# Kernel tuning notes

Measured on AMD Instinct MI355X. Metric: run time of the kernel, lower is better.

The kernel has to match this reference:

```python
import jax, jax.numpy as jnp
import numpy as np

B, C, G, S, R = 8192, 4096, 16, 256, 512  # batch, in_channels, clusters, cluster_size, j_rank


def setup_inputs() -> dict:
    key = jax.random.key(0)
    kx, kw, kb, kp = jax.random.split(key, 4)
    x = jax.random.normal(kx, (B, C), dtype=jnp.float32)
    # per-cluster Linear weights [G, out=R, in=S] and biases [G, R]
    W = jax.random.normal(kw, (G, R, S), dtype=jnp.float32) * (1.0 / np.sqrt(S))
    b = jax.random.normal(kb, (G, R), dtype=jnp.float32) * 0.01
    # arrangements: non-contiguous channel clusters = random permutation split into G groups
    perm = jax.random.permutation(kp, C).reshape(G, S).astype(jnp.int32)
    return {"x": x, "W": W, "b": b, "perm": perm}


def reference(x, W, b, perm):
    # gather each cluster's channels: [B, G, S]
    xg = x[:, perm]
    # batched per-cluster linear (y = x_c @ W_c^T + b_c), then concat along dim 1
    out = jnp.einsum('bgs,grs->bgr', xg, W) + b  # [B, G, R]
    return out.reshape(x.shape[0], G * R)
```

## Files before the change

### kernel.cpp

```cpp
#include <hip/hip_runtime.h>

#define BB 8192
#define CC 4096
#define GG 16
#define SS 256
#define RR 512
#define NN (GG*RR)

typedef __bf16 bf16x8 __attribute__((ext_vector_type(8)));
typedef float  f32x4_t __attribute__((ext_vector_type(4)));

__device__ __forceinline__ unsigned short f2bf(float f){
  union{float f; unsigned int u;} v; v.f = f;
  unsigned int r = (v.u + 0x7FFFu + ((v.u>>16)&1u)) >> 16;
  return (unsigned short)r;
}

__device__ __forceinline__ void gld_lds16(const void* g, void* l){
  __builtin_amdgcn_global_load_lds((const __attribute__((address_space(1))) void*)g,
                                   (__attribute__((address_space(3))) void*)l, 16, 0, 0);
}

__global__ void __launch_bounds__(256) permute_cast_kernel(
    const float* __restrict__ x, const int* __restrict__ perm,
    unsigned short* __restrict__ xp)
{
  __shared__ float row[CC];
  const int tid = threadIdx.x;
  const size_t b = blockIdx.x;
  const float4* xr = (const float4*)(x + b*CC);
  float4* rr = (float4*)row;
  #pragma unroll
  for (int c=0;c<4;++c) rr[c*256+tid] = xr[c*256+tid];
  __syncthreads();
  unsigned short* xo = xp + b*CC;
  #pragma unroll
  for (int c=0;c<2;++c){
    const int j0 = (((c<<8)+tid)<<3);
    const int* pp = perm + j0;
    unsigned int w0 = (unsigned)f2bf(row[pp[0]]) | ((unsigned)f2bf(row[pp[1]])<<16);
    unsigned int w1 = (unsigned)f2bf(row[pp[2]]) | ((unsigned)f2bf(row[pp[3]])<<16);
    unsigned int w2 = (unsigned)f2bf(row[pp[4]]) | ((unsigned)f2bf(row[pp[5]])<<16);
    unsigned int w3 = (unsigned)f2bf(row[pp[6]]) | ((unsigned)f2bf(row[pp[7]])<<16);
    uint4 o; o.x=w0; o.y=w1; o.z=w2; o.w=w3;
    *(uint4*)(xo + j0) = o;
  }
}

__global__ void __launch_bounds__(256) cast_w_kernel(
    const float* __restrict__ W, unsigned short* __restrict__ Wb)
{
  const int i = (blockIdx.x*256 + threadIdx.x)<<3;
  float4 f0 = ((const float4*)(W+i))[0];
  float4 f1 = ((const float4*)(W+i))[1];
  uint4 o;
  o.x = (unsigned)f2bf(f0.x) | ((unsigned)f2bf(f0.y)<<16);
  o.y = (unsigned)f2bf(f0.z) | ((unsigned)f2bf(f0.w)<<16);
  o.z = (unsigned)f2bf(f1.x) | ((unsigned)f2bf(f1.y)<<16);
  o.w = (unsigned)f2bf(f1.z) | ((unsigned)f2bf(f1.w)<<16);
  *(uint4*)(Wb+i) = o;
}

__global__ void __launch_bounds__(256) gemm_kernel(
    const unsigned short* __restrict__ xp, const unsigned short* __restrict__ Wb,
    const float* __restrict__ bias, float* __restrict__ out)
{
  __shared__ unsigned short lA[128*64];
  __shared__ unsigned short lB[128*64];
  const int tid  = threadIdx.x;
  const int lane = tid & 63;
  const int w    = tid >> 6;
  const int wr   = w >> 1, wc = w & 1;
  const int l15  = lane & 15, lh = lane >> 4;

  const int bid   = blockIdx.x;
  const int xcd   = bid & 7;
  const int local = bid >> 3;
  const int bx    = (xcd << 3) + (local & 7);
  const int by    = local >> 3;

  const int m0 = by << 7;
  const int n0 = bx << 7;
  const int g  = bx >> 2;
  const size_t arow0 = (size_t)m0*CC + (size_t)g*SS;
  const size_t brow0 = (size_t)n0*SS;

  f32x4_t acc[4][4];
  for (int i=0;i<4;++i)
    for (int j=0;j<4;++j)
      acc[i][j] = (f32x4_t){0.f,0.f,0.f,0.f};

  for (int kk=0; kk<SS; kk+=64){
    #pragma unroll
    for (int c=0;c<4;++c){
      const int i  = (c<<8) + tid;
      const int r  = i>>3;
      const int cs = ((i&7) ^ (r&7)) << 3;
      gld_lds16(xp + arow0 + (size_t)r*CC + kk + cs, &lA[i<<3]);
      gld_lds16(Wb + brow0 + (size_t)r*SS + kk + cs, &lB[i<<3]);
    }
    __syncthreads();
    #pragma unroll
    for (int ks=0;ks<2;++ks){
      bf16x8 af[4], bfr[4];
      const int cc = (ks<<2) + lh;
      #pragma unroll
      for (int mi=0;mi<4;++mi){
        const int ar = (wr<<6)+(mi<<4)+l15;
        af[mi]  = *(const bf16x8*)&lA[ar*64 + ((cc ^ (ar&7))<<3)];
      }
      #pragma unroll
      for (int ni=0;ni<4;++ni){
        const int br = (wc<<6)+(ni<<4)+l15;
        bfr[ni] = *(const bf16x8*)&lB[br*64 + ((cc ^ (br&7))<<3)];
      }
      #pragma unroll
      for (int mi=0;mi<4;++mi){
        #pragma unroll
        for (int ni=0;ni<4;++ni)
          acc[mi][ni] = __builtin_amdgcn_mfma_f32_16x16x32_bf16(af[mi], bfr[ni], acc[mi][ni], 0,0,0);
      }
    }
    __syncthreads();
  }

  #pragma unroll
  for (int ni=0;ni<4;++ni){
    const int col = n0 + (wc<<6) + (ni<<4) + l15;
    const float bv = bias[col];
    #pragma unroll
    for (int mi=0;mi<4;++mi){
      const int rb = m0 + (wr<<6) + (mi<<4) + (lh<<2);
      float* op = out + (size_t)rb*NN + col;
      #pragma unroll
      for (int r=0;r<4;++r)
        op[(size_t)r*NN] = acc[mi][ni][r] + bv;
    }
  }
}

extern "C" void kernel_launch(void* const* d_in, const int* in_sizes, int n_in,
                              void* d_out, int out_size, void* d_ws, size_t ws_size,
                              hipStream_t stream) {
  const float* x    = (const float*)d_in[0];
  const float* W    = (const float*)d_in[1];
  const float* bias = (const float*)d_in[2];
  const int*   perm = (const int*)d_in[3];
  float* out = (float*)d_out;

  unsigned short* xp = (unsigned short*)d_ws;
  unsigned short* Wb = (unsigned short*)((char*)d_ws + (size_t)BB*CC*2);

  permute_cast_kernel<<<dim3(BB), dim3(256), 0, stream>>>(x, perm, xp);
  cast_w_kernel<<<dim3((GG*RR*SS)/(256*8)), dim3(256), 0, stream>>>(W, Wb);
  gemm_kernel<<<dim3(4096), dim3(256), 0, stream>>>(xp, Wb, bias, out);
}
```

Measured before the change: 137.1 us.

## Double-buffer GEMM LDS tiles with 8 waves and merge prep kernels

Merges the x permute/cast and W cast kernels into one launch by splitting the block index range. The GEMM now uses 512 threads (8 waves, each with a 64x32 sub-tile) and double-buffered LDS, so direct-to-LDS loads for the next K step are issued while the current one computes, synchronised with explicit vmcnt waits and barriers. This aims to hide global load latency and cut one launch. The cost is twice the LDS per block and a fragile hand-counted vmcnt scheme.

Result: faster. 123.8 us (-9.6%).

```diff
diff --git a/kernel.cpp b/kernel.cpp
--- a/kernel.cpp
+++ b/kernel.cpp
@@ -21,56 +21,57 @@
                                    (__attribute__((address_space(3))) void*)l, 16, 0, 0);
 }
 
-__global__ void __launch_bounds__(256) permute_cast_kernel(
+__global__ void __launch_bounds__(256) prep_kernel(
     const float* __restrict__ x, const int* __restrict__ perm,
-    unsigned short* __restrict__ xp)
+    const float* __restrict__ W,
+    unsigned short* __restrict__ xp, unsigned short* __restrict__ Wb)
 {
   __shared__ float row[CC];
   const int tid = threadIdx.x;
-  const size_t b = blockIdx.x;
-  const float4* xr = (const float4*)(x + b*CC);
-  float4* rr = (float4*)row;
-  #pragma unroll
-  for (int c=0;c<4;++c) rr[c*256+tid] = xr[c*256+tid];
-  __syncthreads();
-  unsigned short* xo = xp + b*CC;
-  #pragma unroll
-  for (int c=0;c<2;++c){
-    const int j0 = (((c<<8)+tid)<<3);
-    const int* pp = perm + j0;
-    unsigned int w0 = (unsigned)f2bf(row[pp[0]]) | ((unsigned)f2bf(row[pp[1]])<<16);
-    unsigned int w1 = (unsigned)f2bf(row[pp[2]]) | ((unsigned)f2bf(row[pp[3]])<<16);
-    unsigned int w2 = (unsigned)f2bf(row[pp[4]]) | ((unsigned)f2bf(row[pp[5]])<<16);
-    unsigned int w3 = (unsigned)f2bf(row[pp[6]]) | ((unsigned)f2bf(row[pp[7]])<<16);
-    uint4 o; o.x=w0; o.y=w1; o.z=w2; o.w=w3;
-    *(uint4*)(xo + j0) = o;
+  const int bid = blockIdx.x;
+  if (bid < BB) {
+    const size_t b = bid;
+    const float4* xr = (const float4*)(x + b*CC);
+    float4* rr = (float4*)row;
+    #pragma unroll
+    for (int c=0;c<4;++c) rr[c*256+tid] = xr[c*256+tid];
+    __syncthreads();
+    unsigned short* xo = xp + b*CC;
+    #pragma unroll
+    for (int c=0;c<2;++c){
+      const int j0 = (((c<<8)+tid)<<3);
+      const int* pp = perm + j0;
+      unsigned int w0 = (unsigned)f2bf(row[pp[0]]) | ((unsigned)f2bf(row[pp[1]])<<16);
+      unsigned int w1 = (unsigned)f2bf(row[pp[2]]) | ((unsigned)f2bf(row[pp[3]])<<16);
+      unsigned int w2 = (unsigned)f2bf(row[pp[4]]) | ((unsigned)f2bf(row[pp[5]])<<16);
+      unsigned int w3 = (unsigned)f2bf(row[pp[6]]) | ((unsigned)f2bf(row[pp[7]])<<16);
+      uint4 o; o.x=w0; o.y=w1; o.z=w2; o.w=w3;
+      *(uint4*)(xo + j0) = o;
+    }
+  } else {
+    const int i = (((bid - BB)<<8) + tid)<<3;
+    float4 f0 = ((const float4*)(W+i))[0];
+    float4 f1 = ((const float4*)(W+i))[1];
+    uint4 o;
+    o.x = (unsigned)f2bf(f0.x) | ((unsigned)f2bf(f0.y)<<16);
+    o.y = (unsigned)f2bf(f0.z) | ((unsigned)f2bf(f0.w)<<16);
+    o.z = (unsigned)f2bf(f1.x) | ((unsigned)f2bf(f1.y)<<16);
+    o.w = (unsigned)f2bf(f1.z) | ((unsigned)f2bf(f1.w)<<16);
+    *(uint4*)(Wb+i) = o;
   }
 }
 
-__global__ void __launch_bounds__(256) cast_w_kernel(
-    const float* __restrict__ W, unsigned short* __restrict__ Wb)
-{
-  const int i = (blockIdx.x*256 + threadIdx.x)<<3;
-  float4 f0 = ((const float4*)(W+i))[0];
-  float4 f1 = ((const float4*)(W+i))[1];
-  uint4 o;
-  o.x = (unsigned)f2bf(f0.x) | ((unsigned)f2bf(f0.y)<<16);
-  o.y = (unsigned)f2bf(f0.z) | ((unsigned)f2bf(f0.w)<<16);
-  o.z = (unsigned)f2bf(f1.x) | ((unsigned)f2bf(f1.y)<<16);
-  o.w = (unsigned)f2bf(f1.z) | ((unsigned)f2bf(f1.w)<<16);
-  *(uint4*)(Wb+i) = o;
-}
-
-__global__ void __launch_bounds__(256) gemm_kernel(
+__global__ void __launch_bounds__(512, 4) gemm_kernel(
     const unsigned short* __restrict__ xp, const unsigned short* __restrict__ Wb,
     const float* __restrict__ bias, float* __restrict__ out)
 {
-  __shared__ unsigned short lA[128*64];
-  __shared__ unsigned short lB[128*64];
+  __shared__ unsigned short lA[2][128*64];
+  __shared__ unsigned short lB[2][128*64];
   const int tid  = threadIdx.x;
   const int lane = tid & 63;
   const int w    = tid >> 6;
-  const int wr   = w >> 1, wc = w & 1;
+  const int wr   = w >> 2;
+  const int wc   = w & 3;
   const int l15  = lane & 15, lh = lane >> 4;
 
   const int bid   = blockIdx.x;
@@ -85,48 +86,68 @@
   const size_t arow0 = (size_t)m0*CC + (size_t)g*SS;
   const size_t brow0 = (size_t)n0*SS;
 
-  f32x4_t acc[4][4];
+  f32x4_t acc[4][2];
+  #pragma unroll
   for (int i=0;i<4;++i)
-    for (int j=0;j<4;++j)
+    #pragma unroll
+    for (int j=0;j<2;++j)
       acc[i][j] = (f32x4_t){0.f,0.f,0.f,0.f};
 
-  for (int kk=0; kk<SS; kk+=64){
+  auto STAGE = [&](int kk, int buf){
     #pragma unroll
-    for (int c=0;c<4;++c){
-      const int i  = (c<<8) + tid;
+    for (int c=0;c<2;++c){
+      const int i  = (c<<9) + tid;
       const int r  = i>>3;
       const int cs = ((i&7) ^ (r&7)) << 3;
-      gld_lds16(xp + arow0 + (size_t)r*CC + kk + cs, &lA[i<<3]);
-      gld_lds16(Wb + brow0 + (size_t)r*SS + kk + cs, &lB[i<<3]);
+      gld_lds16(xp + arow0 + (size_t)r*CC + kk + cs, &lA[buf][i<<3]);
     }
-    __syncthreads();
+    #pragma unroll
+    for (int c=0;c<2;++c){
+      const int i  = (c<<9) + tid;
+      const int r  = i>>3;
+      const int cs = ((i&7) ^ (r&7)) << 3;
+      gld_lds16(Wb + brow0 + (size_t)r*SS + kk + cs, &lB[buf][i<<3]);
+    }
+  };
+
+  auto COMPUTE = [&](int buf){
     #pragma unroll
     for (int ks=0;ks<2;++ks){
-      bf16x8 af[4], bfr[4];
+      bf16x8 af[4], bfr[2];
       const int cc = (ks<<2) + lh;
       #pragma unroll
       for (int mi=0;mi<4;++mi){
         const int ar = (wr<<6)+(mi<<4)+l15;
-        af[mi]  = *(const bf16x8*)&lA[ar*64 + ((cc ^ (ar&7))<<3)];
+        af[mi]  = *(const bf16x8*)&lA[buf][ar*64 + ((cc ^ (ar&7))<<3)];
       }
       #pragma unroll
-      for (int ni=0;ni<4;++ni){
-        const int br = (wc<<6)+(ni<<4)+l15;
-        bfr[ni] = *(const bf16x8*)&lB[br*64 + ((cc ^ (br&7))<<3)];
+      for (int ni=0;ni<2;++ni){
+        const int br = (wc<<5)+(ni<<4)+l15;
+        bfr[ni] = *(const bf16x8*)&lB[buf][br*64 + ((cc ^ (br&7))<<3)];
       }
       #pragma unroll
-      for (int mi=0;mi<4;++mi){
+      for (int mi=0;mi<4;++mi)
         #pragma unroll
-        for (int ni=0;ni<4;++ni)
+        for (int ni=0;ni<2;++ni)
           acc[mi][ni] = __builtin_amdgcn_mfma_f32_16x16x32_bf16(af[mi], bfr[ni], acc[mi][ni], 0,0,0);
-      }
     }
-    __syncthreads();
+  };
+
+  STAGE(0, 0);
+  STAGE(64, 1);
+  #pragma unroll
+  for (int t=0;t<4;++t){
+    if (t<3) asm volatile("s_waitcnt vmcnt(4)" ::: "memory");
+    else     asm volatile("s_waitcnt vmcnt(0)" ::: "memory");
+    __builtin_amdgcn_s_barrier();
+    COMPUTE(t&1);
+    __builtin_amdgcn_s_barrier();
+    if (t<2) STAGE((t+2)<<6, t&1);
   }
 
   #pragma unroll
-  for (int ni=0;ni<4;++ni){
-    const int col = n0 + (wc<<6) + (ni<<4) + l15;
+  for (int ni=0;ni<2;++ni){
+    const int col = n0 + (wc<<5) + (ni<<4) + l15;
     const float bv = bias[col];
     #pragma unroll
     for (int mi=0;mi<4;++mi){
@@ -151,7 +172,7 @@
   unsigned short* xp = (unsigned short*)d_ws;
   unsigned short* Wb = (unsigned short*)((char*)d_ws + (size_t)BB*CC*2);
 
-  permute_cast_kernel<<<dim3(BB), dim3(256), 0, stream>>>(x, perm, xp);
-  cast_w_kernel<<<dim3((GG*RR*SS)/(256*8)), dim3(256), 0, stream>>>(W, Wb);
-  gemm_kernel<<<dim3(4096), dim3(256), 0, stream>>>(xp, Wb, bias, out);
+  const int wblocks = (GG*RR*SS)/(256*8);
+  prep_kernel<<<dim3(BB + wblocks), dim3(256), 0, stream>>>(x, perm, W, xp, Wb);
+  gemm_kernel<<<dim3(4096), dim3(512), 0, stream>>>(xp, Wb, bias, out);
 }
```
